# Performance work log

Measured on AMD Instinct MI355X. Metric: run time of the kernel, lower is better.

## Reference

```python
import jax, jax.numpy as jnp
import numpy as np

N1 = 50000        # nodes in g1
N_LAYERS = 3
N2 = N1 * N_LAYERS  # nodes in g2 (kron tiling)
E1 = 800000
E2 = 2400000
D = 64
LEAKY_SLOPE = 0.01


def graph_conv(x, src, dst, num_nodes, W, b):
    """DGL GraphConv with norm='both', in_feats == out_feats (aggregate-then-matmul).
    h = D_in^{-1/2} A D_out^{-1/2} x W + b, degrees clamped to >=1.
    """
    ones_e = jnp.ones(src.shape[0], dtype=x.dtype)
    out_deg = jax.ops.segment_sum(ones_e, src, num_segments=num_nodes)
    in_deg = jax.ops.segment_sum(ones_e, dst, num_segments=num_nodes)
    norm_src = jnp.power(jnp.clip(out_deg, 1.0), -0.5)  # [N]
    norm_dst = jnp.power(jnp.clip(in_deg, 1.0), -0.5)   # [N]
    feat = x * norm_src[:, None]                         # [N, D]
    agg = jax.ops.segment_sum(feat[src], dst, num_segments=num_nodes)  # [N, D]
    rst = agg * norm_dst[:, None]
    return rst @ W + b


def setup_inputs() -> dict:
    key = jax.random.key(0)
    k = jax.random.split(key, 8)
    return {
        "node_features": jax.random.normal(k[0], (N1, D), dtype=jnp.float32),
        "WQ": jax.random.normal(k[1], (D, D), dtype=jnp.float32) * (1.0 / np.sqrt(D)),
        "bQ": jnp.zeros((D,), dtype=jnp.float32),
        "WM": jax.random.normal(k[2], (D, D), dtype=jnp.float32) * (1.0 / np.sqrt(D)),
        "bM": jnp.zeros((D,), dtype=jnp.float32),
        "src1": jax.random.randint(k[3], (E1,), 0, N1, dtype=jnp.int32),
        "dst1": jax.random.randint(k[4], (E1,), 0, N1, dtype=jnp.int32),
        "src2": jax.random.randint(k[5], (E2,), 0, N2, dtype=jnp.int32),
        "dst2": jax.random.randint(k[6], (E2,), 0, N2, dtype=jnp.int32),
    }


def reference(node_features, WQ, bQ, WM, bM, src1, dst1, src2, dst2):
    h_Q1 = graph_conv(node_features, src1, dst1, N1, WQ, bQ)
    h_Q1 = jax.nn.leaky_relu(h_Q1, negative_slope=LEAKY_SLOPE)
    # torch.kron(ones(n_layers,1), h_Q1) == vertical tiling
    M_feat = jnp.tile(h_Q1, (N_LAYERS, 1))  # [N_LAYERS*N1, D]
    h_M1 = graph_conv(M_feat, src2, dst2, N2, WM, bM)
    return jax.nn.leaky_relu(h_M1, negative_slope=LEAKY_SLOPE)
```

## Files before the change

### kernel.cpp

```cpp
#include <hip/hip_runtime.h>
#include <hip/hip_fp16.h>

constexpr int cN1 = 50000;
constexpr int cN2 = 150000;
constexpr int cE1 = 800000;
constexpr int cE2 = 2400000;
constexpr int cD  = 64;
constexpr int MAXB = 640;
#define LEAKY 0.01f

constexpr int NB1 = (cN1 + 255) / 256;
constexpr int NB2 = (cN2 + 255) / 256;

constexpr int BD1 = 64, BD2 = 192, BS1 = 64, BS2 = 192, CVB = 256;
constexpr int PR0 = BD1;
constexpr int PR1 = PR0 + BD2;
constexpr int PR2 = PR1 + BS1;
constexpr int PR3 = PR2 + BS2;
constexpr int PR4 = PR3 + CVB;

constexpr int SD1 = 64, SD2 = 128, SS1 = 32, SS2 = 64;

__device__ __forceinline__ void bucket_count_region(
    const int* __restrict__ idx, int E4, int* __restrict__ bcnt, int nbuck,
    int b, int B, int* h) {
    for (int i = threadIdx.x; i < nbuck; i += 256) h[i] = 0;
    __syncthreads();
    const int4* v4 = (const int4*)idx;
    for (int i = b * 256 + threadIdx.x; i < E4; i += B * 256) {
        int4 v = v4[i];
        atomicAdd(&h[v.x >> 8], 1);
        atomicAdd(&h[v.y >> 8], 1);
        atomicAdd(&h[v.z >> 8], 1);
        atomicAdd(&h[v.w >> 8], 1);
    }
    __syncthreads();
    for (int i = threadIdx.x; i < nbuck; i += 256) {
        int c = h[i];
        if (c) atomicAdd(&bcnt[i], c);
    }
}

__global__ __launch_bounds__(256) void prep_kernel(
    const int* __restrict__ dst1, const int* __restrict__ dst2,
    const int* __restrict__ src1, const int* __restrict__ src2,
    const float* __restrict__ x, __half* __restrict__ xh,
    int* __restrict__ bcntD1, int* __restrict__ bcntD2,
    int* __restrict__ bcntS1, int* __restrict__ bcntS2) {
    __shared__ int h[MAXB];
    int b = blockIdx.x;
    if (b < PR0) {
        bucket_count_region(dst1, cE1 / 4, bcntD1, NB1, b, BD1, h);
    } else if (b < PR1) {
        bucket_count_region(dst2, cE2 / 4, bcntD2, NB2, b - PR0, BD2, h);
    } else if (b < PR2) {
        bucket_count_region(src1, cE1 / 4, bcntS1, NB1, b - PR1, BS1, h);
    } else if (b < PR3) {
        bucket_count_region(src2, cE2 / 4, bcntS2, NB2, b - PR2, BS2, h);
    } else {
        int i = (b - PR3) * 256 + threadIdx.x;
        const int n4 = cN1 * cD / 4;
        for (; i < n4; i += CVB * 256) {
            float4 v = ((const float4*)x)[i];
            __half2* o = (__half2*)xh;
            o[2 * i]     = __floats2half2_rn(v.x, v.y);
            o[2 * i + 1] = __floats2half2_rn(v.z, v.w);
        }
    }
}

__global__ __launch_bounds__(256) void scan4_kernel(
    int* __restrict__ bcntD1, int* __restrict__ bbaseD1, int* __restrict__ bcurD1,
    int* __restrict__ bcntD2, int* __restrict__ bbaseD2, int* __restrict__ bcurD2,
    int* __restrict__ bcntS1, int* __restrict__ bbaseS1, int* __restrict__ bcurS1,
    int* __restrict__ bcntS2, int* __restrict__ bbaseS2, int* __restrict__ bcurS2,
    int* __restrict__ offs1, int* __restrict__ offs2) {
    int b = blockIdx.x;
    int tid = threadIdx.x;
    int* bcnt; int* bbase; int* bcur; int n; int e;
    if (b == 0)      { bcnt = bcntD1; bbase = bbaseD1; bcur = bcurD1; n = NB1; e = cE1; }
    else if (b == 1) { bcnt = bcntD2; bbase = bbaseD2; bcur = bcurD2; n = NB2; e = cE2; }
    else if (b == 2) { bcnt = bcntS1; bbase = bbaseS1; bcur = bcurS1; n = NB1; e = cE1; }
    else             { bcnt = bcntS2; bbase = bbaseS2; bcur = bcurS2; n = NB2; e = cE2; }
    if (b == 0 && tid == 0) offs1[cN1] = cE1;
    if (b == 1 && tid == 0) offs2[cN2] = cE2;
    __shared__ int s[256];
    int v[4];
    int t = 0;
#pragma unroll
    for (int j = 0; j < 4; ++j) { int i = tid * 4 + j; v[j] = (i < n) ? bcnt[i] : 0; t += v[j]; }
    s[tid] = t; __syncthreads();
    for (int off = 1; off < 256; off <<= 1) {
        int a = (tid >= off) ? s[tid - off] : 0;
        __syncthreads();
        s[tid] += a;
        __syncthreads();
    }
    int run = s[tid] - t;
#pragma unroll
    for (int j = 0; j < 4; ++j) {
        int i = tid * 4 + j;
        if (i < n) { bbase[i] = run; bcur[i] = run; run += v[j]; }
    }
    if (tid == 0) bbase[n] = e;
}

__global__ __launch_bounds__(1024) void scatter4_kernel(
    const int* __restrict__ src1, const int* __restrict__ dst1,
    int* __restrict__ bcurD1, unsigned int* __restrict__ pairs1,
    const int* __restrict__ src2, const int* __restrict__ dst2,
    int* __restrict__ bcurD2, unsigned int* __restrict__ pairs2,
    int* __restrict__ bcurS1, unsigned char* __restrict__ sval1,
    int* __restrict__ bcurS2, unsigned char* __restrict__ sval2) {
    __shared__ int hist[MAXB];
    __shared__ int cur[MAXB];
    int tid = threadIdx.x;
    int bx = blockIdx.x;
    bool pairMode;
    const int* key; const int* pay; int* bcur;
    unsigned int* pout = nullptr; unsigned char* bout = nullptr;
    int nbuck, E, blk, nblk;
    if (bx < SD1) {
        pairMode = true;  key = dst1; pay = src1; bcur = bcurD1; pout = pairs1;
        nbuck = NB1; E = cE1; blk = bx; nblk = SD1;
    } else if (bx < SD1 + SD2) {
        pairMode = true;  key = dst2; pay = src2; bcur = bcurD2; pout = pairs2;
        nbuck = NB2; E = cE2; blk = bx - SD1; nblk = SD2;
    } else if (bx < SD1 + SD2 + SS1) {
        pairMode = false; key = src1; pay = nullptr; bcur = bcurS1; bout = sval1;
        nbuck = NB1; E = cE1; blk = bx - SD1 - SD2; nblk = SS1;
    } else {
        pairMode = false; key = src2; pay = nullptr; bcur = bcurS2; bout = sval2;
        nbuck = NB2; E = cE2; blk = bx - SD1 - SD2 - SS1; nblk = SS2;
    }
    int spe = (((E / 4) + nblk - 1) / nblk) * 4;
    int b0 = blk * spe;
    int b1 = b0 + spe; if (b1 > E) b1 = E;
    for (int i = tid; i < nbuck; i += 1024) hist[i] = 0;
    __syncthreads();
    for (int i = b0 + tid * 4; i < b1; i += 4096) {
        int4 d = *(const int4*)(key + i);
        atomicAdd(&hist[d.x >> 8], 1);
        atomicAdd(&hist[d.y >> 8], 1);
        atomicAdd(&hist[d.z >> 8], 1);
        atomicAdd(&hist[d.w >> 8], 1);
    }
    __syncthreads();
    for (int i = tid; i < nbuck; i += 1024) cur[i] = atomicAdd(&bcur[i], hist[i]);
    __syncthreads();
    if (pairMode) {
        for (int i = b0 + tid * 4; i < b1; i += 4096) {
            int4 d = *(const int4*)(key + i);
            int4 s = *(const int4*)(pay + i);
            int p0 = atomicAdd(&cur[d.x >> 8], 1);
            pout[p0] = ((unsigned)(d.x & 255) << 24) | (unsigned)s.x;
            int p1 = atomicAdd(&cur[d.y >> 8], 1);
            pout[p1] = ((unsigned)(d.y & 255) << 24) | (unsigned)s.y;
            int p2 = atomicAdd(&cur[d.z >> 8], 1);
            pout[p2] = ((unsigned)(d.z & 255) << 24) | (unsigned)s.z;
            int p3 = atomicAdd(&cur[d.w >> 8], 1);
            pout[p3] = ((unsigned)(d.w & 255) << 24) | (unsigned)s.w;
        }
    } else {
        for (int i = b0 + tid * 4; i < b1; i += 4096) {
            int4 d = *(const int4*)(key + i);
            int p0 = atomicAdd(&cur[d.x >> 8], 1); bout[p0] = (unsigned char)(d.x & 255);
            int p1 = atomicAdd(&cur[d.y >> 8], 1); bout[p1] = (unsigned char)(d.y & 255);
            int p2 = atomicAdd(&cur[d.z >> 8], 1); bout[p2] = (unsigned char)(d.z & 255);
            int p3 = atomicAdd(&cur[d.w >> 8], 1); bout[p3] = (unsigned char)(d.w & 255);
        }
    }
}

__global__ __launch_bounds__(256) void sbin_kernel(
    const unsigned char* __restrict__ sval1, const int* __restrict__ bbaseS1,
    float* __restrict__ nsrc1,
    const unsigned char* __restrict__ sval2, const int* __restrict__ bbaseS2,
    float* __restrict__ nsrc2) {
    const unsigned char* sv; const int* bbase; float* nsrc; int N, bk;
    if (blockIdx.x < NB1) { sv = sval1; bbase = bbaseS1; nsrc = nsrc1; N = cN1; bk = blockIdx.x; }
    else                  { sv = sval2; bbase = bbaseS2; nsrc = nsrc2; N = cN2; bk = blockIdx.x - NB1; }
    __shared__ int cnt[256];
    int tid = threadIdx.x;
    cnt[tid] = 0;
    __syncthreads();
    int k0 = bbase[bk];
    int k1 = bbase[bk + 1];
    for (int k = k0 + tid; k < k1; k += 256) atomicAdd(&cnt[sv[k]], 1);
    __syncthreads();
    int lo = bk << 8;
    int span = N - lo; if (span > 256) span = 256;
    if (tid < span) {
        int d = cnt[tid];
        d = d < 1 ? 1 : d;
        nsrc[lo + tid] = rsqrtf((float)d);
    }
}

__global__ __launch_bounds__(256) void bin12_kernel(
    const unsigned int* __restrict__ pairs1, const int* __restrict__ bbase1,
    const float* __restrict__ nsrc1, unsigned int* __restrict__ sorted1,
    int* __restrict__ offs1,
    const unsigned int* __restrict__ pairs2, const int* __restrict__ bbase2,
    const float* __restrict__ nsrc2, unsigned int* __restrict__ sorted2,
    int* __restrict__ offs2) {
    const unsigned int* pairs; const int* bbase; const float* nsrc;
    unsigned int* sorted; int* offs; int N, foldn, bk;
    if (blockIdx.x < NB1) {
        pairs = pairs1; bbase = bbase1; nsrc = nsrc1; sorted = sorted1;
        offs = offs1; N = cN1; foldn = 0; bk = blockIdx.x;
    } else {
        pairs = pairs2; bbase = bbase2; nsrc = nsrc2; sorted = sorted2;
        offs = offs2; N = cN2; foldn = cN1; bk = blockIdx.x - NB1;
    }
    __shared__ int cnt[256];
    __shared__ int s[256];
    __shared__ int cur[256];
    int tid = threadIdx.x;
    int lo = bk << 8;
    int span = N - lo; if (span > 256) span = 256;
    int k0 = bbase[bk];
    int k1 = bbase[bk + 1];
    cnt[tid] = 0;
    __syncthreads();
    for (int k = k0 + tid; k < k1; k += 256) atomicAdd(&cnt[pairs[k] >> 24], 1);
    __syncthreads();
    int v = cnt[tid];
    s[tid] = v; __syncthreads();
    for (int off = 1; off < 256; off <<= 1) {
        int a = (tid >= off) ? s[tid - off] : 0;
        __syncthreads();
        s[tid] += a;
        __syncthreads();
    }
    int excl = s[tid] - v;
    cur[tid] = k0 + excl;
    if (tid < span) offs[lo + tid] = k0 + excl;
    __syncthreads();
    for (int k = k0 + tid; k < k1; k += 256) {
        unsigned pr = pairs[k];
        int d = pr >> 24;
        int sidx = (int)(pr & 0xFFFFFFu);
        int r = sidx;
        if (foldn) {
            if (r >= 2 * foldn) r -= 2 * foldn;
            else if (r >= foldn) r -= foldn;
        }
        __half nh = __float2half(nsrc[sidx]);
        int pos = atomicAdd(&cur[d], 1);
        sorted[pos] = ((unsigned)__half_as_ushort(nh) << 16) | (unsigned)r;
    }
}

#define FMA8(v, nv)                                                     \
    {                                                                   \
        float2 f0 = __half22float2(*(const __half2*)&(v).x);            \
        float2 f1 = __half22float2(*(const __half2*)&(v).y);            \
        float2 f2 = __half22float2(*(const __half2*)&(v).z);            \
        float2 f3 = __half22float2(*(const __half2*)&(v).w);            \
        a0.x = fmaf(f0.x, nv, a0.x); a0.y = fmaf(f0.y, nv, a0.y);       \
        a0.z = fmaf(f1.x, nv, a0.z); a0.w = fmaf(f1.y, nv, a0.w);       \
        a1.x = fmaf(f2.x, nv, a1.x); a1.y = fmaf(f2.y, nv, a1.y);       \
        a1.z = fmaf(f3.x, nv, a1.z); a1.w = fmaf(f3.y, nv, a1.w);       \
    }

template <bool EPI>
__global__ __launch_bounds__(256) void agg_csr_kernel(
    const __half* __restrict__ feat, const unsigned int* __restrict__ sorted,
    const int* __restrict__ offs, float* __restrict__ outp,
    const float* __restrict__ bias, int N) {
    int w = (blockIdx.x * blockDim.x + threadIdx.x) >> 4;
    if (w >= N) return;
    int l16  = threadIdx.x & 15;
    int slot = l16 >> 3;
    int c    = l16 & 7;

    int k0 = offs[w];
    int k1 = offs[w + 1];
    float4 a0 = {0.f, 0.f, 0.f, 0.f};
    float4 a1 = {0.f, 0.f, 0.f, 0.f};

    int k = k0 + slot;
    for (; k + 2 < k1; k += 4) {
        unsigned eA = sorted[k];
        unsigned eB = sorted[k + 2];
        float nA = __half2float(__ushort_as_half((unsigned short)(eA >> 16)));
        float nB = __half2float(__ushort_as_half((unsigned short)(eB >> 16)));
        int rA = (int)(eA & 0xFFFFu);
        int rB = (int)(eB & 0xFFFFu);
        uint4 vA = *(const uint4*)(feat + (size_t)rA * cD + c * 8);
        uint4 vB = *(const uint4*)(feat + (size_t)rB * cD + c * 8);
        FMA8(vA, nA);
        FMA8(vB, nB);
    }
    if (k < k1) {
        unsigned e = sorted[k];
        float nv = __half2float(__ushort_as_half((unsigned short)(e >> 16)));
        int r = (int)(e & 0xFFFFu);
        uint4 v = *(const uint4*)(feat + (size_t)r * cD + c * 8);
        FMA8(v, nv);
    }

    a0.x += __shfl_xor(a0.x, 8); a0.y += __shfl_xor(a0.y, 8);
    a0.z += __shfl_xor(a0.z, 8); a0.w += __shfl_xor(a0.w, 8);
    a1.x += __shfl_xor(a1.x, 8); a1.y += __shfl_xor(a1.y, 8);
    a1.z += __shfl_xor(a1.z, 8); a1.w += __shfl_xor(a1.w, 8);

    if (slot == 0) {
        if (EPI) {
            int dg = k1 - k0;
            float nd = rsqrtf((float)(dg < 1 ? 1 : dg));
            float4 b0 = *(const float4*)(bias + c * 8);
            float4 b1 = *(const float4*)(bias + c * 8 + 4);
            float4 r0, r1;
            r0.x = fmaf(a0.x, nd, b0.x); r0.y = fmaf(a0.y, nd, b0.y);
            r0.z = fmaf(a0.z, nd, b0.z); r0.w = fmaf(a0.w, nd, b0.w);
            r1.x = fmaf(a1.x, nd, b1.x); r1.y = fmaf(a1.y, nd, b1.y);
            r1.z = fmaf(a1.z, nd, b1.z); r1.w = fmaf(a1.w, nd, b1.w);
            r0.x = r0.x > 0.f ? r0.x : LEAKY * r0.x;
            r0.y = r0.y > 0.f ? r0.y : LEAKY * r0.y;
            r0.z = r0.z > 0.f ? r0.z : LEAKY * r0.z;
            r0.w = r0.w > 0.f ? r0.w : LEAKY * r0.w;
            r1.x = r1.x > 0.f ? r1.x : LEAKY * r1.x;
            r1.y = r1.y > 0.f ? r1.y : LEAKY * r1.y;
            r1.z = r1.z > 0.f ? r1.z : LEAKY * r1.z;
            r1.w = r1.w > 0.f ? r1.w : LEAKY * r1.w;
            *(float4*)(outp + (size_t)w * cD + c * 8) = r0;
            *(float4*)(outp + (size_t)w * cD + c * 8 + 4) = r1;
        } else {
            *(float4*)(outp + (size_t)w * cD + c * 8) = a0;
            *(float4*)(outp + (size_t)w * cD + c * 8 + 4) = a1;
        }
    }
}
#undef FMA8

constexpr int GR = 32;
constexpr int RP = 36;

__global__ __launch_bounds__(256) void gemm12_kernel(
    const float* __restrict__ A, const int* __restrict__ offs,
    const float* __restrict__ WQ_, const float* __restrict__ bQ_,
    const float* __restrict__ WM_, __half* __restrict__ g, int N) {
    __shared__ float W1s[64 * 64];
    __shared__ float W2s[64 * 64];
    __shared__ float Rs_t[64 * RP];
    __shared__ float Hs_t[64 * RP];
    __shared__ float rn_s[GR];
    int tid = threadIdx.x;
    int row0 = blockIdx.x * GR;

    for (int i = tid; i < 64 * 64; i += 256) {
        W1s[i] = WQ_[i];
        W2s[i] = WM_[i];
    }
    if (tid < GR) {
        int row = row0 + tid;
        if (row < N) {
            int dg = offs[row + 1] - offs[row];
            rn_s[tid] = rsqrtf((float)(dg < 1 ? 1 : dg));
        } else {
            rn_s[tid] = 0.f;
        }
    }
    __syncthreads();
    for (int i = tid; i < GR * 64; i += 256) {
        int r = i >> 6;
        int k = i & 63;
        int row = row0 + r;
        float v = (row < N) ? A[(size_t)row * cD + k] * rn_s[r] : 0.f;
        Rs_t[k * RP + r] = v;
    }
    __syncthreads();

    int j  = tid & 63;
    int gq = tid >> 6;
    int r0 = gq * 8;

    float acc[8];
    float bq = bQ_[j];
#pragma unroll
    for (int i = 0; i < 8; ++i) acc[i] = bq;
#pragma unroll 8
    for (int k = 0; k < 64; ++k) {
        float wv = W1s[k * 64 + j];
        float4 ra = *(const float4*)&Rs_t[k * RP + r0];
        float4 rb = *(const float4*)&Rs_t[k * RP + r0 + 4];
        acc[0] = fmaf(ra.x, wv, acc[0]); acc[1] = fmaf(ra.y, wv, acc[1]);
        acc[2] = fmaf(ra.z, wv, acc[2]); acc[3] = fmaf(ra.w, wv, acc[3]);
        acc[4] = fmaf(rb.x, wv, acc[4]); acc[5] = fmaf(rb.y, wv, acc[5]);
        acc[6] = fmaf(rb.z, wv, acc[6]); acc[7] = fmaf(rb.w, wv, acc[7]);
    }
    float4 h0, h1;
    h0.x = acc[0] > 0.f ? acc[0] : LEAKY * acc[0];
    h0.y = acc[1] > 0.f ? acc[1] : LEAKY * acc[1];
    h0.z = acc[2] > 0.f ? acc[2] : LEAKY * acc[2];
    h0.w = acc[3] > 0.f ? acc[3] : LEAKY * acc[3];
    h1.x = acc[4] > 0.f ? acc[4] : LEAKY * acc[4];
    h1.y = acc[5] > 0.f ? acc[5] : LEAKY * acc[5];
    h1.z = acc[6] > 0.f ? acc[6] : LEAKY * acc[6];
    h1.w = acc[7] > 0.f ? acc[7] : LEAKY * acc[7];
    *(float4*)&Hs_t[j * RP + r0]     = h0;
    *(float4*)&Hs_t[j * RP + r0 + 4] = h1;
    __syncthreads();

    float acc2[8];
#pragma unroll
    for (int i = 0; i < 8; ++i) acc2[i] = 0.f;
#pragma unroll 8
    for (int k = 0; k < 64; ++k) {
        float wv = W2s[k * 64 + j];
        float4 ra = *(const float4*)&Hs_t[k * RP + r0];
        float4 rb = *(const float4*)&Hs_t[k * RP + r0 + 4];
        acc2[0] = fmaf(ra.x, wv, acc2[0]); acc2[1] = fmaf(ra.y, wv, acc2[1]);
        acc2[2] = fmaf(ra.z, wv, acc2[2]); acc2[3] = fmaf(ra.w, wv, acc2[3]);
        acc2[4] = fmaf(rb.x, wv, acc2[4]); acc2[5] = fmaf(rb.y, wv, acc2[5]);
        acc2[6] = fmaf(rb.z, wv, acc2[6]); acc2[7] = fmaf(rb.w, wv, acc2[7]);
    }
#pragma unroll
    for (int i = 0; i < 8; ++i) {
        int row = row0 + r0 + i;
        if (row < N) g[(size_t)row * cD + j] = __float2half(acc2[i]);
    }
}

extern "C" void kernel_launch(void* const* d_in, const int* in_sizes, int n_in,
                              void* d_out, int out_size, void* d_ws, size_t ws_size,
                              hipStream_t stream) {
    const float* x    = (const float*)d_in[0];
    const float* WQ   = (const float*)d_in[1];
    const float* bQ   = (const float*)d_in[2];
    const float* WM   = (const float*)d_in[3];
    const float* bM   = (const float*)d_in[4];
    const int*   src1 = (const int*)d_in[5];
    const int*   dst1 = (const int*)d_in[6];
    const int*   src2 = (const int*)d_in[7];
    const int*   dst2 = (const int*)d_in[8];
    float* out = (float*)d_out;

    char* p = (char*)d_ws;
    int*    bcntD1 = (int*)p;    p += sizeof(int) * MAXB;
    int*    bcntD2 = (int*)p;    p += sizeof(int) * MAXB;
    int*    bcntS1 = (int*)p;    p += sizeof(int) * MAXB;
    int*    bcntS2 = (int*)p;    p += sizeof(int) * MAXB;
    int*    bbaseD1= (int*)p;    p += sizeof(int) * (MAXB + 1);
    int*    bbaseD2= (int*)p;    p += sizeof(int) * (MAXB + 1);
    int*    bbaseS1= (int*)p;    p += sizeof(int) * (MAXB + 1);
    int*    bbaseS2= (int*)p;    p += sizeof(int) * (MAXB + 1);
    int*    bcurD1 = (int*)p;    p += sizeof(int) * MAXB;
    int*    bcurD2 = (int*)p;    p += sizeof(int) * MAXB;
    int*    bcurS1 = (int*)p;    p += sizeof(int) * MAXB;
    int*    bcurS2 = (int*)p;    p += sizeof(int) * MAXB;
    float*  nsrc1  = (float*)p;  p += sizeof(float) * cN1;
    float*  nsrc2  = (float*)p;  p += sizeof(float) * cN2;
    int*    offs1  = (int*)p;    p += sizeof(int) * (cN1 + 1);
    int*    offs2  = (int*)p;    p += sizeof(int) * (cN2 + 1);
    unsigned int* sorted2 = (unsigned int*)p; p += sizeof(int) * cE2;
    __half* gh     = (__half*)p; p += sizeof(__half) * (size_t)cN1 * cD;

    int* dout_i = (int*)d_out;
    unsigned int*  pairs2  = (unsigned int*)dout_i;
    unsigned int*  pairs1  = (unsigned int*)(dout_i + cE2);
    __half*        xh      = (__half*)(dout_i + cE2 + cE1);
    float*         agg1buf = (float*)(dout_i + cE2 + cE1 + (size_t)cN1 * cD / 2);
    unsigned char* sval2   = (unsigned char*)(dout_i + 8000000);
    unsigned char* sval1   = (unsigned char*)(dout_i + 8600000);
    unsigned int*  sorted1 = (unsigned int*)(dout_i + ((size_t)cN2 * cD - cE1));

    hipMemsetAsync(bcntD1, 0, sizeof(int) * 4 * MAXB, stream);

    prep_kernel<<<PR4, 256, 0, stream>>>(dst1, dst2, src1, src2, x, xh,
                                         bcntD1, bcntD2, bcntS1, bcntS2);

    scan4_kernel<<<4, 256, 0, stream>>>(
        bcntD1, bbaseD1, bcurD1, bcntD2, bbaseD2, bcurD2,
        bcntS1, bbaseS1, bcurS1, bcntS2, bbaseS2, bcurS2, offs1, offs2);

    scatter4_kernel<<<SD1 + SD2 + SS1 + SS2, 1024, 0, stream>>>(
        src1, dst1, bcurD1, pairs1, src2, dst2, bcurD2, pairs2,
        bcurS1, sval1, bcurS2, sval2);

    sbin_kernel<<<NB1 + NB2, 256, 0, stream>>>(
        sval1, bbaseS1, nsrc1, sval2, bbaseS2, nsrc2);

    bin12_kernel<<<NB1 + NB2, 256, 0, stream>>>(
        pairs1, bbaseD1, nsrc1, sorted1, offs1,
        pairs2, bbaseD2, nsrc2, sorted2, offs2);

    agg_csr_kernel<false><<<(cN1 + 15) / 16, 256, 0, stream>>>(
        xh, sorted1, offs1, agg1buf, nullptr, cN1);
    gemm12_kernel<<<(cN1 + GR - 1) / GR, 256, 0, stream>>>(
        agg1buf, offs1, WQ, bQ, WM, gh, cN1);

    agg_csr_kernel<true><<<(cN2 + 15) / 16, 256, 0, stream>>>(
        gh, sorted2, offs2, out, bM, cN2);
}
```

Before: 215.6 us.

## Split CSR aggregation into two column-half passes with more edge-parallel slots

The aggregation kernel now handles 32 of the 64 feature columns per launch, and each launch covers one column half. Within a 16-lane group, 4 lanes cover the columns and 4 slots process edges in parallel instead of 2. This halves the gathered bytes per pass, which may improve cache locality for the random feature gathers and raise memory-level parallelism per node. In exchange, the edge list and offsets are read twice, launch count doubles, and an extra shuffle reduction stage is added.

New measurement: 248.2 us. 1.15x slower.

```diff
diff --git a/kernel.cpp b/kernel.cpp
--- a/kernel.cpp
+++ b/kernel.cpp
@@ -268,12 +268,12 @@
 __global__ __launch_bounds__(256) void agg_csr_kernel(
     const __half* __restrict__ feat, const unsigned int* __restrict__ sorted,
     const int* __restrict__ offs, float* __restrict__ outp,
-    const float* __restrict__ bias, int N) {
+    const float* __restrict__ bias, int N, int colOff) {
     int w = (blockIdx.x * blockDim.x + threadIdx.x) >> 4;
     if (w >= N) return;
     int l16  = threadIdx.x & 15;
-    int slot = l16 >> 3;
-    int c    = l16 & 7;
+    int slot = l16 >> 2;
+    int c    = l16 & 3;
 
     int k0 = offs[w];
     int k1 = offs[w + 1];
@@ -281,15 +281,15 @@
     float4 a1 = {0.f, 0.f, 0.f, 0.f};
 
     int k = k0 + slot;
-    for (; k + 2 < k1; k += 4) {
+    for (; k + 4 < k1; k += 8) {
         unsigned eA = sorted[k];
-        unsigned eB = sorted[k + 2];
+        unsigned eB = sorted[k + 4];
         float nA = __half2float(__ushort_as_half((unsigned short)(eA >> 16)));
         float nB = __half2float(__ushort_as_half((unsigned short)(eB >> 16)));
         int rA = (int)(eA & 0xFFFFu);
         int rB = (int)(eB & 0xFFFFu);
-        uint4 vA = *(const uint4*)(feat + (size_t)rA * cD + c * 8);
-        uint4 vB = *(const uint4*)(feat + (size_t)rB * cD + c * 8);
+        uint4 vA = *(const uint4*)(feat + (size_t)rA * cD + colOff + c * 8);
+        uint4 vB = *(const uint4*)(feat + (size_t)rB * cD + colOff + c * 8);
         FMA8(vA, nA);
         FMA8(vB, nB);
     }
@@ -297,10 +297,14 @@
         unsigned e = sorted[k];
         float nv = __half2float(__ushort_as_half((unsigned short)(e >> 16)));
         int r = (int)(e & 0xFFFFu);
-        uint4 v = *(const uint4*)(feat + (size_t)r * cD + c * 8);
+        uint4 v = *(const uint4*)(feat + (size_t)r * cD + colOff + c * 8);
         FMA8(v, nv);
     }
 
+    a0.x += __shfl_xor(a0.x, 4); a0.y += __shfl_xor(a0.y, 4);
+    a0.z += __shfl_xor(a0.z, 4); a0.w += __shfl_xor(a0.w, 4);
+    a1.x += __shfl_xor(a1.x, 4); a1.y += __shfl_xor(a1.y, 4);
+    a1.z += __shfl_xor(a1.z, 4); a1.w += __shfl_xor(a1.w, 4);
     a0.x += __shfl_xor(a0.x, 8); a0.y += __shfl_xor(a0.y, 8);
     a0.z += __shfl_xor(a0.z, 8); a0.w += __shfl_xor(a0.w, 8);
     a1.x += __shfl_xor(a1.x, 8); a1.y += __shfl_xor(a1.y, 8);
@@ -310,8 +314,8 @@
         if (EPI) {
             int dg = k1 - k0;
             float nd = rsqrtf((float)(dg < 1 ? 1 : dg));
-            float4 b0 = *(const float4*)(bias + c * 8);
-            float4 b1 = *(const float4*)(bias + c * 8 + 4);
+            float4 b0 = *(const float4*)(bias + colOff + c * 8);
+            float4 b1 = *(const float4*)(bias + colOff + c * 8 + 4);
             float4 r0, r1;
             r0.x = fmaf(a0.x, nd, b0.x); r0.y = fmaf(a0.y, nd, b0.y);
             r0.z = fmaf(a0.z, nd, b0.z); r0.w = fmaf(a0.w, nd, b0.w);
@@ -325,11 +329,11 @@
             r1.y = r1.y > 0.f ? r1.y : LEAKY * r1.y;
             r1.z = r1.z > 0.f ? r1.z : LEAKY * r1.z;
             r1.w = r1.w > 0.f ? r1.w : LEAKY * r1.w;
-            *(float4*)(outp + (size_t)w * cD + c * 8) = r0;
-            *(float4*)(outp + (size_t)w * cD + c * 8 + 4) = r1;
+            *(float4*)(outp + (size_t)w * cD + colOff + c * 8) = r0;
+            *(float4*)(outp + (size_t)w * cD + colOff + c * 8 + 4) = r1;
         } else {
-            *(float4*)(outp + (size_t)w * cD + c * 8) = a0;
-            *(float4*)(outp + (size_t)w * cD + c * 8 + 4) = a1;
+            *(float4*)(outp + (size_t)w * cD + colOff + c * 8) = a0;
+            *(float4*)(outp + (size_t)w * cD + colOff + c * 8 + 4) = a1;
         }
     }
 }
@@ -487,11 +491,17 @@
         pairs1, bbaseD1, nsrc1, sorted1, offs1,
         pairs2, bbaseD2, nsrc2, sorted2, offs2);
 
-    agg_csr_kernel<false><<<(cN1 + 15) / 16, 256, 0, stream>>>(
-        xh, sorted1, offs1, agg1buf, nullptr, cN1);
+    const int agB1 = (cN1 + 15) / 16;
+    agg_csr_kernel<false><<<agB1, 256, 0, stream>>>(
+        xh, sorted1, offs1, agg1buf, nullptr, cN1, 0);
+    agg_csr_kernel<false><<<agB1, 256, 0, stream>>>(
+        xh, sorted1, offs1, agg1buf, nullptr, cN1, 32);
     gemm12_kernel<<<(cN1 + GR - 1) / GR, 256, 0, stream>>>(
         agg1buf, offs1, WQ, bQ, WM, gh, cN1);
 
-    agg_csr_kernel<true><<<(cN2 + 15) / 16, 256, 0, stream>>>(
-        gh, sorted2, offs2, out, bM, cN2);
-}
+    const int agB2 = (cN2 + 15) / 16;
+    agg_csr_kernel<true><<<agB2, 256, 0, stream>>>(
+        gh, sorted2, offs2, out, bM, cN2, 0);
+    agg_csr_kernel<true><<<agB2, 256, 0, stream>>>(
+        gh, sorted2, offs2, out, bM, cN2, 32);
+}
```
